# Performance work log

Measured on AMD Instinct MI355X. Metric: run time of the kernel, lower is better.

Reference implementation:

```python
import jax, jax.numpy as jnp
import numpy as np

A, B, M, H, E, N = 1, 32, 32, 1024, 8, 1024

def setup_inputs() -> dict:
    key = jax.random.key(0)
    k1, k2, k3 = jax.random.split(key, 3)
    hidden_4d = jax.random.normal(k1, (A, B, M, H), dtype=jnp.float32)
    sparsity = jax.random.uniform(k2, (A, B, 1, E), dtype=jnp.float32)
    weight = jax.random.normal(k3, (1, E, H, N), dtype=jnp.float32) * 0.02
    return {"hidden_4d": hidden_4d, "sparsity": sparsity, "weight": weight}

def reference(hidden_4d, sparsity, weight):
    # Original: out = einsum('abmh,ehn->abemn'); out *= mask[a,b,e,1,1]; out.sum((-2,-1))
    # The mask is constant over (m, n), so the sum fuses into the contraction:
    # contracted[a,b,e] = sum_{m,h,n} hidden[a,b,m,h] * weight[e,h,n]
    contracted = jnp.einsum('abmh,ehn->abe', hidden_4d, weight[0])  # (A,B,E)
    mask = jnp.squeeze(sparsity, axis=2)  # (A,B,E)
    return contracted * mask
```

## Files before the change

kernel.cpp:

```cpp
#include <hip/hip_runtime.h>


#define Bdim 32
#define Mdim 32
#define Hdim 1024
#define Edim 8
#define Ndim 1024

__global__ __launch_bounds__(256) void reduce_kernel(
    const float* __restrict__ hidden,
    const float* __restrict__ weight,
    float* __restrict__ ws)
{
    const int wave = threadIdx.x >> 6;
    const int lane = threadIdx.x & 63;

    {
        const float4* w4 = reinterpret_cast<const float4*>(weight);
        #pragma unroll
        for (int r = 0; r < 4; ++r) {
            const int row = blockIdx.x * 16 + wave * 4 + r;
            float s = 0.f;
            #pragma unroll
            for (int j = 0; j < 4; ++j) {
                float4 v = w4[row * (Ndim / 4) + j * 64 + lane];
                s += (v.x + v.y) + (v.z + v.w);
            }
            #pragma unroll
            for (int off = 32; off > 0; off >>= 1)
                s += __shfl_xor(s, off, 64);
            if (lane == 0) ws[row] = s;
        }
    }

    if (threadIdx.x < 64) {
        const int c  = blockIdx.x * 16 + (lane & 15);
        const int mg = lane >> 4;
        const int b  = c >> 8;
        const int h4 = c & 255;
        const float4* hp = reinterpret_cast<const float4*>(hidden)
                         + b * (Mdim * Hdim / 4) + h4;
        float4 s = {0.f, 0.f, 0.f, 0.f};
        #pragma unroll
        for (int m = 0; m < 8; ++m) {
            float4 v = hp[(mg * 8 + m) * (Hdim / 4)];
            s.x += v.x; s.y += v.y; s.z += v.z; s.w += v.w;
        }
        #pragma unroll
        for (int off = 16; off <= 32; off <<= 1) {
            s.x += __shfl_xor(s.x, off, 64);
            s.y += __shfl_xor(s.y, off, 64);
            s.z += __shfl_xor(s.z, off, 64);
            s.w += __shfl_xor(s.w, off, 64);
        }
        if (mg == 0)
            reinterpret_cast<float4*>(ws + Edim * Hdim)[c] = s;
    }
}

__global__ __launch_bounds__(256) void dot_kernel(
    const float* __restrict__ ws,
    const float* __restrict__ sparsity,
    float* __restrict__ out)
{
    const int o = blockIdx.x * 4 + (threadIdx.x >> 6);
    const int lane = threadIdx.x & 63;
    const int b = o >> 3;
    const int e = o & 7;
    const float4* hs = reinterpret_cast<const float4*>(ws + Edim * Hdim + b * Hdim);
    const float4* wv = reinterpret_cast<const float4*>(ws + e * Hdim);
    float s = 0.f;
    #pragma unroll
    for (int j = 0; j < 4; ++j) {
        float4 h4 = hs[j * 64 + lane];
        float4 w4 = wv[j * 64 + lane];
        s += h4.x * w4.x + h4.y * w4.y + h4.z * w4.z + h4.w * w4.w;
    }
    #pragma unroll
    for (int off = 32; off > 0; off >>= 1)
        s += __shfl_xor(s, off, 64);
    if (lane == 0) out[o] = s * sparsity[o];
}

extern "C" void kernel_launch(void* const* d_in, const int* in_sizes, int n_in,
                              void* d_out, int out_size, void* d_ws, size_t ws_size,
                              hipStream_t stream) {
    const float* hidden   = (const float*)d_in[0];
    const float* sparsity = (const float*)d_in[1];
    const float* weight   = (const float*)d_in[2];
    float* out = (float*)d_out;
    float* ws  = (float*)d_ws;

    reduce_kernel<<<512, 256, 0, stream>>>(hidden, weight, ws);
    dot_kernel<<<64, 256, 0, stream>>>(ws, sparsity, out);
}
```

Baseline: 80.64 us.

## Fuse reduce and dot kernels using an atomic arrival counter grid barrier

Merges the two launches into one kernel. Each block bumps a global atomic counter once it has written its partial sums. The last 64 blocks to arrive (ranks 448–511 within each group of 512) spin until all 512 blocks have arrived, then compute the final dot products and apply the sparsity mask. This is meant to remove the second launch and the gap between kernels. In exchange it adds atomics, a spin-wait tail, and a dependence on workspace contents persisting across calls, since the counter is never reset and the guard word at GUARD_W is only read, never written.

```diff
diff --git a/kernel.cpp b/kernel.cpp
--- a/kernel.cpp
+++ b/kernel.cpp
@@ -7,13 +7,20 @@
 #define Edim 8
 #define Ndim 1024
 
-__global__ __launch_bounds__(256) void reduce_kernel(
+#define CNT_W   40960
+#define GUARD_W 40992
+
+__global__ __launch_bounds__(256) void fused1(
     const float* __restrict__ hidden,
     const float* __restrict__ weight,
+    const float* __restrict__ sparsity,
+    float* __restrict__ out,
     float* __restrict__ ws)
 {
     const int wave = threadIdx.x >> 6;
     const int lane = threadIdx.x & 63;
+    unsigned int* const cnt = reinterpret_cast<unsigned int*>(ws) + CNT_W;
+    const unsigned int g = reinterpret_cast<const unsigned int*>(ws)[GUARD_W];
 
     {
         const float4* w4 = reinterpret_cast<const float4*>(weight);
@@ -56,15 +63,29 @@
         if (mg == 0)
             reinterpret_cast<float4*>(ws + Edim * Hdim)[c] = s;
     }
-}
 
-__global__ __launch_bounds__(256) void dot_kernel(
-    const float* __restrict__ ws,
-    const float* __restrict__ sparsity,
-    float* __restrict__ out)
-{
-    const int o = blockIdx.x * 4 + (threadIdx.x >> 6);
-    const int lane = threadIdx.x & 63;
+    __shared__ unsigned int rel_s;
+    __syncthreads();
+    if (threadIdx.x == 0) {
+        __threadfence();
+        rel_s = atomicAdd(cnt, 1u) - g;
+    }
+    __syncthreads();
+    const unsigned int rel  = rel_s;
+    const unsigned int rank = rel & 511u;
+    if (rank < 448u) return;
+
+    if (threadIdx.x == 0) {
+        const unsigned int target = (rel & ~511u) + 512u;
+        while (__hip_atomic_load(cnt, __ATOMIC_ACQUIRE,
+                                 __HIP_MEMORY_SCOPE_AGENT) - g < target) {
+            __builtin_amdgcn_s_sleep(8);
+        }
+    }
+    __syncthreads();
+    __threadfence();
+
+    const int o = (int)(rank - 448u) * 4 + wave;
     const int b = o >> 3;
     const int e = o & 7;
     const float4* hs = reinterpret_cast<const float4*>(ws + Edim * Hdim + b * Hdim);
@@ -91,6 +112,5 @@
     float* out = (float*)d_out;
     float* ws  = (float*)d_ws;
 
-    reduce_kernel<<<512, 256, 0, stream>>>(hidden, weight, ws);
-    dot_kernel<<<64, 256, 0, stream>>>(ws, sparsity, out);
+    fused1<<<512, 256, 0, stream>>>(hidden, weight, sparsity, out, ws);
 }
```

After: 104.7 us. +29.8%, slower.
